# Kernel tuning notes

Measured on AMD Instinct MI355X. Metric: run time of the kernel, lower is better.

Reference implementation:

```python
import jax, jax.numpy as jnp
import numpy as np
from jax import lax

R = 1          # box-filter radius
EPS = 1e-06    # regularizer


def boxfilter(z, r=R):
    """ReplicationPad2d(r) + depthwise (groups=C) mean conv with kernel (2r+1)^2."""
    k = 2 * r + 1
    c = z.shape[1]
    zp = jnp.pad(z, ((0, 0), (0, 0), (r, r), (r, r)), mode='edge')  # replication pad
    w = jnp.full((c, 1, k, k), 1.0 / (k * k), dtype=z.dtype)        # [O, I/g, kh, kw]
    return lax.conv_general_dilated(zp, w, window_strides=(1, 1), padding='VALID',
                                    feature_group_count=c)


def setup_inputs() -> dict:
    key = jax.random.key(0)
    kx, ky = jax.random.split(key)
    shape = (8, 3, 1024, 1024)
    # image-valued inputs in [0, 255), matching the final clamp range
    x = jax.random.uniform(kx, shape, jnp.float32, 0.0, 255.0)
    y = jax.random.uniform(ky, shape, jnp.float32, 0.0, 255.0)
    return {"x": x, "y": y}


def reference(x, y):
    mean_x = boxfilter(x)
    mean_y = boxfilter(y)
    cov_xy = boxfilter(x * y) - mean_x * mean_y
    var_x = boxfilter(x * x) - mean_x * mean_x
    A = cov_xy / (var_x + EPS)
    b = mean_y - A * mean_x
    res = boxfilter(A) * x + boxfilter(b)
    # torch: res.int() truncates toward zero, clamp(0,255), back to float
    return jnp.clip(jnp.trunc(res), 0.0, 255.0)
```

## Files before the change

kernel.cpp:

```cpp
#include <hip/hip_runtime.h>


#define TH 32
#define OW 60

__global__ __launch_bounds__(256) void gf_kernel(
    const float* __restrict__ xg, const float* __restrict__ yg,
    float* __restrict__ outg, int H, int W) {
  const int lane = threadIdx.x;
  const int img = blockIdx.z;
  const size_t ibase = (size_t)img * H * W;
  const float* __restrict__ xi = xg + ibase;
  const float* __restrict__ yi = yg + ibase;
  float* __restrict__ oi = outg + ibase;

  int tx0 = blockIdx.x * OW;
  if (tx0 > W - OW) tx0 = W - OW;
  const int ty0 = (blockIdx.y * 4 + threadIdx.y) * TH;

  const int col = tx0 + lane - 2;
  const int gxc = min(max(col, 0), W - 1);
  const bool wok = (lane >= 2) && (lane < 62);

  const bool leftE = (tx0 == 0);
  const bool rightE = (tx0 + OW >= W);
  const bool needfix = leftE || rightE;
  int fixsrc = lane;
  if (leftE && lane == 1) fixsrc = 2;
  if (rightE && lane == 62) fixsrc = 61;

  const float inv9 = 1.0f / 9.0f;

  float hA0 = 0.f, hA1 = 0.f, hA2 = 0.f;
  float hB0 = 0.f, hB1 = 0.f, hB2 = 0.f;

  auto step = [&](int ly, bool emit) {
    int cy = min(max(ty0 + ly - 1, 0), H - 1);
    int r0 = max(cy - 1, 0);
    int r2 = min(cy + 1, H - 1);
    const float* xr0 = xi + (size_t)r0 * W;
    const float* xr1 = xi + (size_t)cy * W;
    const float* xr2 = xi + (size_t)r2 * W;
    const float* yr0 = yi + (size_t)r0 * W;
    const float* yr1 = yi + (size_t)cy * W;
    const float* yr2 = yi + (size_t)r2 * W;
    float xa = xr0[gxc], xb = xr1[gxc], xc = xr2[gxc];
    float ya = yr0[gxc], yb = yr1[gxc], yc = yr2[gxc];

    float vx = xa + xb + xc;
    float vy = ya + yb + yc;
    float vxy = xa * ya + xb * yb + xc * yc;
    float vxx = xa * xa + xb * xb + xc * xc;

    float Sx  = __shfl_up(vx, 1)  + vx  + __shfl_down(vx, 1);
    float Sy  = __shfl_up(vy, 1)  + vy  + __shfl_down(vy, 1);
    float Sxy = __shfl_up(vxy, 1) + vxy + __shfl_down(vxy, 1);
    float Sxx = __shfl_up(vxx, 1) + vxx + __shfl_down(vxx, 1);

    float num = 9.0f * Sxy - Sx * Sy;
    float den = 9.0f * Sxx - Sx * Sx + 8.1e-05f;
    float rden;
    asm("v_rcp_f32 %0, %1" : "=v"(rden) : "v"(den));
    float A = num * rden;
    float b = Sy * inv9 - A * (Sx * inv9);

    if (needfix) {
      A = __shfl(A, fixsrc);
      b = __shfl(b, fixsrc);
    }

    float hAn = __shfl_up(A, 1) + A + __shfl_down(A, 1);
    float hBn = __shfl_up(b, 1) + b + __shfl_down(b, 1);
    hA0 = hA1; hA1 = hA2; hA2 = hAn;
    hB0 = hB1; hB1 = hB2; hB2 = hBn;

    if (emit) {
      int gr = ty0 + ly - 2;
      float xv = (r0 == gr) ? xa : xb;
      float SA = hA0 + hA1 + hA2;
      float SB = hB0 + hB1 + hB2;
      float res = (SA * xv + SB) * inv9;
      float t = truncf(res);
      t = fminf(fmaxf(t, 0.0f), 255.0f);
      if (wok) oi[(size_t)gr * W + col] = t;
    }
  };

  step(0, false);
  step(1, false);
#pragma unroll 4
  for (int ly = 2; ly < TH + 2; ++ly) step(ly, true);
}

extern "C" void kernel_launch(void* const* d_in, const int* in_sizes, int n_in,
                              void* d_out, int out_size, void* d_ws, size_t ws_size,
                              hipStream_t stream) {
  const float* x = (const float*)d_in[0];
  const float* y = (const float*)d_in[1];
  float* out = (float*)d_out;
  const int H = 1024, W = 1024;
  const int imgs = in_sizes[0] / (H * W);
  dim3 block(64, 4, 1);
  dim3 grid((W + OW - 1) / OW, H / (TH * 4), imgs);
  gf_kernel<<<grid, block, 0, stream>>>(x, y, out, H, W);
}
```

Before: 297.1 us.

## Process four columns per lane with float4 loads and register row reuse

Each lane now handles four adjacent columns using vector loads, so a wave covers 248 output columns instead of 60. The earlier 3x reload of each input row is replaced by a rolling register window with one-row prefetch. The change also adds nontemporal vector stores and an occupancy hint. Together these cut redundant global loads, halo overhead and shuffle count per output, at the cost of more registers and trickier edge handling for replication at the image borders.

```diff
diff --git a/kernel.cpp b/kernel.cpp
--- a/kernel.cpp
+++ b/kernel.cpp
@@ -1,10 +1,12 @@
 #include <hip/hip_runtime.h>
 
 
+typedef float f4 __attribute__((ext_vector_type(4)));
+
 #define TH 32
-#define OW 60
+#define OWPB 248
 
-__global__ __launch_bounds__(256) void gf_kernel(
+__global__ __launch_bounds__(256, 4) void gf_kernel(
     const float* __restrict__ xg, const float* __restrict__ yg,
     float* __restrict__ outg, int H, int W) {
   const int lane = threadIdx.x;
@@ -14,82 +16,129 @@
   const float* __restrict__ yi = yg + ibase;
   float* __restrict__ oi = outg + ibase;
 
-  int tx0 = blockIdx.x * OW;
-  if (tx0 > W - OW) tx0 = W - OW;
+  int tx0 = blockIdx.x * OWPB;
+  const int skipb = tx0;
+  if (tx0 > W - OWPB) tx0 = W - OWPB;
   const int ty0 = (blockIdx.y * 4 + threadIdx.y) * TH;
 
-  const int col = tx0 + lane - 2;
-  const int gxc = min(max(col, 0), W - 1);
-  const bool wok = (lane >= 2) && (lane < 62);
-
+  const int c0 = tx0 - 4 + 4 * lane;
+  const bool inb = (c0 >= 0) && (c0 <= W - 4);
+  const int cbc = (c0 < 0) ? 0 : (W - 1);
+  const bool wok = (lane >= 1) && (lane <= 62) && (c0 >= skipb);
   const bool leftE = (tx0 == 0);
-  const bool rightE = (tx0 + OW >= W);
-  const bool needfix = leftE || rightE;
-  int fixsrc = lane;
-  if (leftE && lane == 1) fixsrc = 2;
-  if (rightE && lane == 62) fixsrc = 61;
-
+  const bool rightE = (tx0 + OWPB >= W);
   const float inv9 = 1.0f / 9.0f;
 
-  float hA0 = 0.f, hA1 = 0.f, hA2 = 0.f;
-  float hB0 = 0.f, hB1 = 0.f, hB2 = 0.f;
+  f4 xr0, xr1, xr2, yr0, yr1, yr2, xpf, ypf;
+  f4 hA0, hA1, hA2, hA3, hB0, hB1, hB2, hB3;
+  int nextr;
 
-  auto step = [&](int ly, bool emit) {
-    int cy = min(max(ty0 + ly - 1, 0), H - 1);
-    int r0 = max(cy - 1, 0);
-    int r2 = min(cy + 1, H - 1);
-    const float* xr0 = xi + (size_t)r0 * W;
-    const float* xr1 = xi + (size_t)cy * W;
-    const float* xr2 = xi + (size_t)r2 * W;
-    const float* yr0 = yi + (size_t)r0 * W;
-    const float* yr1 = yi + (size_t)cy * W;
-    const float* yr2 = yi + (size_t)r2 * W;
-    float xa = xr0[gxc], xb = xr1[gxc], xc = xr2[gxc];
-    float ya = yr0[gxc], yb = yr1[gxc], yc = yr2[gxc];
-
-    float vx = xa + xb + xc;
-    float vy = ya + yb + yc;
-    float vxy = xa * ya + xb * yb + xc * yc;
-    float vxx = xa * xa + xb * xb + xc * xc;
-
-    float Sx  = __shfl_up(vx, 1)  + vx  + __shfl_down(vx, 1);
-    float Sy  = __shfl_up(vy, 1)  + vy  + __shfl_down(vy, 1);
-    float Sxy = __shfl_up(vxy, 1) + vxy + __shfl_down(vxy, 1);
-    float Sxx = __shfl_up(vxx, 1) + vxx + __shfl_down(vxx, 1);
-
-    float num = 9.0f * Sxy - Sx * Sy;
-    float den = 9.0f * Sxx - Sx * Sx + 8.1e-05f;
-    float rden;
-    asm("v_rcp_f32 %0, %1" : "=v"(rden) : "v"(den));
-    float A = num * rden;
-    float b = Sy * inv9 - A * (Sx * inv9);
-
-    if (needfix) {
-      A = __shfl(A, fixsrc);
-      b = __shfl(b, fixsrc);
-    }
-
-    float hAn = __shfl_up(A, 1) + A + __shfl_down(A, 1);
-    float hBn = __shfl_up(b, 1) + b + __shfl_down(b, 1);
-    hA0 = hA1; hA1 = hA2; hA2 = hAn;
-    hB0 = hB1; hB1 = hB2; hB2 = hBn;
-
-    if (emit) {
-      int gr = ty0 + ly - 2;
-      float xv = (r0 == gr) ? xa : xb;
-      float SA = hA0 + hA1 + hA2;
-      float SB = hB0 + hB1 + hB2;
-      float res = (SA * xv + SB) * inv9;
-      float t = truncf(res);
-      t = fminf(fmaxf(t, 0.0f), 255.0f);
-      if (wok) oi[(size_t)gr * W + col] = t;
+  auto ldrow = [&](int r, f4& xv, f4& yv) {
+    const float* xr = xi + (size_t)r * W;
+    const float* yr = yi + (size_t)r * W;
+    if (inb) {
+      xv = *(const f4*)(xr + c0);
+      yv = *(const f4*)(yr + c0);
+    } else {
+      float a = xr[cbc], b = yr[cbc];
+      xv = (f4)(a);
+      yv = (f4)(b);
     }
   };
 
-  step(0, false);
-  step(1, false);
+  auto hsum3 = [&](f4 v) {
+    float vl = __shfl_up(v[3], 1);
+    float vr = __shfl_down(v[0], 1);
+    float a01 = v[0] + v[1], a12 = v[1] + v[2], a23 = v[2] + v[3];
+    f4 s;
+    s[0] = vl + a01;
+    s[1] = a01 + v[2];
+    s[2] = a12 + v[3];
+    s[3] = a23 + vr;
+    return s;
+  };
+
+  auto emit_row = [&](int ly, f4 xv) {
+    f4 SA = hA1 + hA2 + hA3;
+    f4 SB = hB1 + hB2 + hB3;
+    f4 st;
+#pragma unroll
+    for (int j = 0; j < 4; ++j) {
+      float res = (SA[j] * xv[j] + SB[j]) * inv9;
+      float t = truncf(res);
+      st[j] = fminf(fmaxf(t, 0.0f), 255.0f);
+    }
+    if (wok) {
+      int gr = ty0 + ly - 2;
+      __builtin_nontemporal_store(st, (f4*)(oi + (size_t)gr * W + c0));
+    }
+  };
+
+  auto dup_hist = [&]() {
+    hA0 = hA1; hA1 = hA2; hA2 = hA3;
+    hB0 = hB1; hB1 = hB2; hB2 = hB3;
+  };
+
+  auto step_adv = [&](int ly, bool doemit, bool dopf) {
+    xr0 = xr1; xr1 = xr2; xr2 = xpf;
+    yr0 = yr1; yr1 = yr2; yr2 = ypf;
+    if (dopf) {
+      ldrow(nextr, xpf, ypf);
+      nextr = min(nextr + 1, H - 1);
+    }
+    f4 vx = xr0 + xr1 + xr2;
+    f4 vy = yr0 + yr1 + yr2;
+    f4 vxy = xr0 * yr0 + xr1 * yr1 + xr2 * yr2;
+    f4 vxx = xr0 * xr0 + xr1 * xr1 + xr2 * xr2;
+    f4 Sx = hsum3(vx), Sy = hsum3(vy), Sxy = hsum3(vxy), Sxx = hsum3(vxx);
+    f4 A, B;
+#pragma unroll
+    for (int j = 0; j < 4; ++j) {
+      float num = 9.0f * Sxy[j] - Sx[j] * Sy[j];
+      float den = 9.0f * Sxx[j] - Sx[j] * Sx[j] + 8.1e-05f;
+      float rd;
+      asm("v_rcp_f32 %0, %1" : "=v"(rd) : "v"(den));
+      float a = num * rd;
+      A[j] = a;
+      B[j] = Sy[j] * inv9 - a * (Sx[j] * inv9);
+    }
+    if (leftE) {
+      float ta = __shfl_down(A[0], 1), tb = __shfl_down(B[0], 1);
+      if (lane == 0) { A[3] = ta; B[3] = tb; }
+    }
+    if (rightE) {
+      float ta = __shfl_up(A[3], 1), tb = __shfl_up(B[3], 1);
+      if (lane == 63) { A[0] = ta; B[0] = tb; }
+    }
+    f4 hAn = hsum3(A), hBn = hsum3(B);
+    hA0 = hA1; hA1 = hA2; hA2 = hA3; hA3 = hAn;
+    hB0 = hB1; hB1 = hB2; hB2 = hB3; hB3 = hBn;
+    if (doemit) emit_row(ly, xr0);
+  };
+
+  {
+    int cy0 = max(ty0 - 1, 0);
+    int ra = max(cy0 - 1, 0);
+    ldrow(ra, xr1, yr1);
+    ldrow(cy0, xr2, yr2);
+    nextr = min(cy0 + 1, H - 1);
+    ldrow(nextr, xpf, ypf);
+    nextr = min(nextr + 1, H - 1);
+  }
+  hA0 = hA1 = hA2 = hA3 = (f4)(0.0f);
+  hB0 = hB1 = hB2 = hB3 = (f4)(0.0f);
+
+  step_adv(0, false, true);
+  if (ty0 == 0) dup_hist();
+  else step_adv(1, false, true);
 #pragma unroll 4
-  for (int ly = 2; ly < TH + 2; ++ly) step(ly, true);
+  for (int ly = 2; ly <= TH; ++ly) step_adv(ly, true, true);
+  if (ty0 == H - TH) {
+    dup_hist();
+    emit_row(TH + 1, xr1);
+  } else {
+    step_adv(TH + 1, true, false);
+  }
 }
 
 extern "C" void kernel_launch(void* const* d_in, const int* in_sizes, int n_in,
@@ -101,6 +150,6 @@
   const int H = 1024, W = 1024;
   const int imgs = in_sizes[0] / (H * W);
   dim3 block(64, 4, 1);
-  dim3 grid((W + OW - 1) / OW, H / (TH * 4), imgs);
+  dim3 grid((W + OWPB - 1) / OWPB, H / (TH * 4), imgs);
   gf_kernel<<<grid, block, 0, stream>>>(x, y, out, H, W);
 }
```

Result: faster. 266.8 us (-10.2%).
